# Performance work log

Hardware: AMD Instinct MI355X
Metric: run time of the kernel (lower is better)

## Reference

```python
import jax, jax.numpy as jnp
import numpy as np

B, S, D, H = 4, 2048, 1024, 16
DH = D // H


def setup_inputs() -> dict:
    key = jax.random.key(0)
    ks = jax.random.split(key, 12)
    s = 0.02
    inp = {
        "q": jax.random.normal(ks[0], (B, S, D), jnp.float32),
        "k": jax.random.normal(ks[1], (B, S, D), jnp.float32),
        "v": jax.random.normal(ks[2], (B, S, D), jnp.float32),
        # causal mask, broadcastable over batch and heads (mask==0 -> -1e9)
        "mask": jnp.tril(jnp.ones((S, S), jnp.int32))[None, None, :, :],
        "wq": jax.random.normal(ks[3], (D, D), jnp.float32) * s,
        "bq": jnp.zeros((D,), jnp.float32),
        "wk": jax.random.normal(ks[4], (D, D), jnp.float32) * s,
        "bk": jnp.zeros((D,), jnp.float32),
        "wv": jax.random.normal(ks[5], (D, D), jnp.float32) * s,
        "bv": jnp.zeros((D,), jnp.float32),
        "wo": jax.random.normal(ks[6], (D, D), jnp.float32) * s,
        "bo": jnp.zeros((D,), jnp.float32),
    }
    return inp


def reference(q, k, v, mask, wq, bq, wk, bk, wv, bv, wo, bo):
    # linear projections (torch Linear: x @ W^T + b)
    qh = (q @ wq.T + bq).reshape(B, S, H, DH).transpose(0, 2, 1, 3)  # [B,H,S,DH]
    kh = (k @ wk.T + bk).reshape(B, S, H, DH).transpose(0, 2, 1, 3)
    vh = (v @ wv.T + bv).reshape(B, S, H, DH).transpose(0, 2, 1, 3)
    scale = 1.0 / jnp.sqrt(jnp.float32(DH))
    score = jnp.einsum("bhqd,bhkd->bhqk", qh, kh) * scale  # [B,H,S,S]
    score = jnp.where(mask == 0, jnp.float32(-1e9), score)
    attn = jax.nn.softmax(score, axis=-1)
    ctx = jnp.einsum("bhqk,bhkd->bhqd", attn, vh)  # [B,H,S,DH]
    ctx = ctx.transpose(0, 2, 1, 3).reshape(B, S, D)
    return ctx @ wo.T + bo
```

## Files before the change

kernel.cpp:

```cpp
#include <hip/hip_runtime.h>
#include <hip/hip_bf16.h>

#define NB 4
#define NS 2048
#define ND 1024
#define NH 16
#define NDH 64
#define E_ 8388608
#define W_ 1048576

typedef __attribute__((ext_vector_type(8))) __bf16 bf16x8;
typedef __attribute__((ext_vector_type(4))) float f32x4;
typedef __attribute__((ext_vector_type(2))) unsigned int u32x2;
typedef unsigned short us16;
typedef unsigned int u32;

__device__ __forceinline__ unsigned short f2bf(float f) {
  union { float f; unsigned u; } v; v.f = f;
  unsigned r = v.u + 0x7FFFu + ((v.u >> 16) & 1u);
  return (unsigned short)(r >> 16);
}

typedef const __attribute__((address_space(1))) unsigned int* gas_t;
typedef __attribute__((address_space(3))) unsigned int* las_t;
__device__ __forceinline__ void gl2lds16(const void* g, void* l) {
  __builtin_amdgcn_global_load_lds((gas_t)g, (las_t)l, 16, 0, 0);
}

__global__ __launch_bounds__(256) void conv_bf16(
    const float* __restrict__ q, const float* __restrict__ k, const float* __restrict__ v,
    const float* __restrict__ wq, const float* __restrict__ wk, const float* __restrict__ wv,
    const float* __restrict__ wo,
    us16* __restrict__ qb, us16* __restrict__ kb, us16* __restrict__ vb,
    us16* __restrict__ wqb, us16* __restrict__ wkb, us16* __restrict__ wvb,
    us16* __restrict__ wob)
{
  int b = blockIdx.x;
  int seg, off;
  if (b < 24576) { seg = b >> 13; off = b & 8191; }
  else { b -= 24576; seg = 3 + (b >> 10); off = b & 1023; }
  const float* s; us16* d;
  switch (seg) {
    case 0: s = q;  d = qb;  break;
    case 1: s = k;  d = kb;  break;
    case 2: s = v;  d = vb;  break;
    case 3: s = wq; d = wqb; break;
    case 4: s = wk; d = wkb; break;
    case 5: s = wv; d = wvb; break;
    default: s = wo; d = wob; break;
  }
  size_t idx = ((size_t)off * 256 + threadIdx.x) * 4;
  float4 f = *(const float4*)(s + idx);
  ushort4 u;
  u.x = f2bf(f.x); u.y = f2bf(f.y); u.z = f2bf(f.z); u.w = f2bf(f.w);
  *(ushort4*)(d + idx) = u;
}

__global__ __launch_bounds__(256, 3) void gemm_qv(
    const us16* __restrict__ A0, const us16* __restrict__ A1,
    const us16* __restrict__ W0, const us16* __restrict__ W1,
    const float* __restrict__ bias0, const float* __restrict__ bias1,
    us16* __restrict__ out0, us16* __restrict__ out1, float scale)
{
  const int z = blockIdx.z;
  const us16* A  = z ? A1 : A0;
  const us16* Wt = z ? W1 : W0;
  const float* bias = z ? bias1 : bias0;

  __shared__ us16 As[128][64];
  __shared__ us16 Bs[128][64];
  const int tid = threadIdx.x;
  const int lane = tid & 63;
  const int w = tid >> 6;
  const int l15 = lane & 15, quad = lane >> 4;
  const int sw = l15 & 7;
  const int rowBase = blockIdx.x * 128, colBase = blockIdx.y * 128;
  const int srow = w * 32 + (lane >> 3);
  const int cu = (lane & 7) ^ ((lane >> 3) & 7);
  const us16* ga = A  + (size_t)(rowBase + srow) * ND + cu * 8;
  const us16* gb = Wt + (size_t)(colBase + srow) * ND + cu * 8;
  const int wr = (w >> 1) * 64, wc = (w & 1) * 64;

  f32x4 acc[4][4] = {};
  for (int kt = 0; kt < ND; kt += 64) {
    __syncthreads();
    #pragma unroll
    for (int c = 0; c < 4; ++c) {
      gl2lds16(ga + kt + c * 8 * ND, &As[w * 32 + c * 8][0]);
      gl2lds16(gb + kt + c * 8 * ND, &Bs[w * 32 + c * 8][0]);
    }
    __syncthreads();
    #pragma unroll
    for (int ks = 0; ks < 2; ++ks) {
      bf16x8 af[4], bfr[4];
      #pragma unroll
      for (int i = 0; i < 4; ++i)
        af[i]  = *(const bf16x8*)&As[wr + i * 16 + l15][((ks * 4 + quad) ^ sw) * 8];
      #pragma unroll
      for (int j = 0; j < 4; ++j)
        bfr[j] = *(const bf16x8*)&Bs[wc + j * 16 + l15][((ks * 4 + quad) ^ sw) * 8];
      #pragma unroll
      for (int i = 0; i < 4; ++i)
        #pragma unroll
        for (int j = 0; j < 4; ++j)
          acc[i][j] = __builtin_amdgcn_mfma_f32_16x16x32_bf16(af[i], bfr[j], acc[i][j], 0, 0, 0);
    }
  }

  if (z == 0) {
    #pragma unroll
    for (int i = 0; i < 4; ++i) {
      #pragma unroll
      for (int j = 0; j < 4; ++j) {
        int colg = colBase + wc + j * 16 + l15;
        float bval = bias[colg];
        #pragma unroll
        for (int r = 0; r < 4; ++r) {
          int rowg = rowBase + wr + i * 16 + quad * 4 + r;
          out0[(size_t)rowg * ND + colg] = f2bf((acc[i][j][r] + bval) * scale);
        }
      }
    }
  } else {
    #pragma unroll
    for (int i = 0; i < 4; ++i) {
      #pragma unroll
      for (int j = 0; j < 4; ++j) {
        int colg = colBase + wc + j * 16 + l15;
        float bval = bias[colg];
        int h_ = colg >> 6, d_ = colg & 63;
        int rowg0 = rowBase + wr + i * 16 + quad * 4;
        int b_ = rowg0 >> 11, s0 = rowg0 & (NS - 1);
        ushort4 vv;
        vv.x = f2bf(acc[i][j][0] + bval);
        vv.y = f2bf(acc[i][j][1] + bval);
        vv.z = f2bf(acc[i][j][2] + bval);
        vv.w = f2bf(acc[i][j][3] + bval);
        *(ushort4*)(out1 + ((size_t)(b_ * NH + h_) * NDH + d_) * NS + s0) = vv;
      }
    }
  }
}

__global__ __launch_bounds__(256, 4) void attn(
    const us16* __restrict__ Qh, const us16* __restrict__ Kh,
    const us16* __restrict__ Vht, us16* __restrict__ ctx)
{
  __shared__ us16 Ks[2][64][64];
  __shared__ us16 Vts[2][64][64];
  __shared__ us16 Ps[4][32][32];
  us16* Qsta = &Vts[0][0][0];

  const int bh = blockIdx.x >> 3;
  const int pr = blockIdx.x & 7;
  const int b_ = bh >> 4, h_ = bh & 15;
  const int tid = threadIdx.x, lane = tid & 63, w = tid >> 6;
  const int l15 = lane & 15, quad = lane >> 4;
  const int sw = l15 & 7;
  const int lr8 = lane >> 3;
  const int cu = (lane & 7) ^ (lr8 & 7);

  bf16x8 ones;
  #pragma unroll
  for (int i = 0; i < 8; ++i) ones[i] = (__bf16)1.0f;

  const us16* gkbase = Kh  + ((size_t)b_ * NS + w * 16 + lr8) * ND + h_ * NDH + cu * 8;
  const us16* gvbase = Vht + ((size_t)bh * NDH + w * 16 + lr8) * NS + cu * 8;

  for (int pass = 0; pass < 2; ++pass) {
    const int tq = pass ? (15 - pr) : pr;
    const int qb0 = tq * 128;
    const int nt = tq * 2 + 2;
    const int qw = qb0 + w * 32;

    __syncthreads();
    {
      const us16* gq = Qh + ((size_t)b_ * NS + qb0 + w * 32 + lr8) * ND + h_ * NDH + cu * 8;
      #pragma unroll
      for (int u = 0; u < 4; ++u)
        gl2lds16(gq + (size_t)u * 8 * ND, Qsta + (w * 32 + u * 8) * 64);
    }
    __syncthreads();
    bf16x8 bq[2][2];
    #pragma unroll
    for (int ntl = 0; ntl < 2; ++ntl)
      #pragma unroll
      for (int c = 0; c < 2; ++c)
        bq[ntl][c] = *(const bf16x8*)(Qsta + (w * 32 + ntl * 16 + l15) * 64 +
                                      (((c * 4 + quad) ^ sw) * 8));
    __syncthreads();

    gl2lds16(gkbase,            &Ks[0][w * 16][0]);
    gl2lds16(gkbase + 8 * ND,   &Ks[0][w * 16 + 8][0]);
    gl2lds16(gvbase,            &Vts[0][w * 16][0]);
    gl2lds16(gvbase + 8 * NS,   &Vts[0][w * 16 + 8][0]);

    f32x4 o[2][4] = {};
    f32x4 o_l[2] = {};

    for (int it = 0; it < nt; ++it) {
      const int kb = it * 64;
      const int cur = it & 1;
      __syncthreads();
      if (it + 1 < nt) {
        const int nxt = cur ^ 1;
        gl2lds16(gkbase + (size_t)(kb + 64) * ND,          &Ks[nxt][w * 16][0]);
        gl2lds16(gkbase + (size_t)(kb + 72) * ND,          &Ks[nxt][w * 16 + 8][0]);
        gl2lds16(gvbase + kb + 64,                         &Vts[nxt][w * 16][0]);
        gl2lds16(gvbase + kb + 64 + 8 * NS,                &Vts[nxt][w * 16 + 8][0]);
      }
      if (kb <= qw + 31) {
        const bool full = (kb + 63 <= qw);
        #pragma unroll
        for (int h2 = 0; h2 < 2; ++h2) {
          f32x4 s[2][2];
          #pragma unroll
          for (int mt = 0; mt < 2; ++mt) {
            bf16x8 ak0 = *(const bf16x8*)&Ks[cur][h2 * 32 + mt * 16 + l15][(quad ^ sw) * 8];
            bf16x8 ak1 = *(const bf16x8*)&Ks[cur][h2 * 32 + mt * 16 + l15][((4 + quad) ^ sw) * 8];
            #pragma unroll
            for (int ntl = 0; ntl < 2; ++ntl) {
              f32x4 t = {};
              t = __builtin_amdgcn_mfma_f32_16x16x32_bf16(ak0, bq[ntl][0], t, 0, 0, 0);
              t = __builtin_amdgcn_mfma_f32_16x16x32_bf16(ak1, bq[ntl][1], t, 0, 0, 0);
              s[mt][ntl] = t;
            }
          }
          #pragma unroll
          for (int mt = 0; mt < 2; ++mt)
            #pragma unroll
            for (int ntl = 0; ntl < 2; ++ntl) {
              u32 u[4];
              if (full) {
                #pragma unroll
                for (int r = 0; r < 4; ++r)
                  u[r] = __float_as_uint(__builtin_amdgcn_exp2f(s[mt][ntl][r]));
              } else {
                const int keyb = kb + h2 * 32 + mt * 16 + quad * 4;
                const int qg = qw + ntl * 16 + l15;
                #pragma unroll
                for (int r = 0; r < 4; ++r) {
                  float p = (keyb + r <= qg) ? __builtin_amdgcn_exp2f(s[mt][ntl][r]) : 0.f;
                  u[r] = __float_as_uint(p);
                }
              }
              u32 lo = (u[0] >> 16) | (u[1] & 0xffff0000u);
              u32 hi = (u[2] >> 16) | (u[3] & 0xffff0000u);
              int uswz = (mt * 2 + (quad >> 1)) ^ (l15 & 3);
              *(u32x2*)&Ps[w][ntl * 16 + l15][uswz * 8 + (quad & 1) * 4] = (u32x2){lo, hi};
            }
          #pragma unroll
          for (int ntl = 0; ntl < 2; ++ntl) {
            bf16x8 ap = *(const bf16x8*)&Ps[w][ntl * 16 + l15][(quad ^ (l15 & 3)) * 8];
            o_l[ntl] = __builtin_amdgcn_mfma_f32_16x16x32_bf16(ap, ones, o_l[ntl], 0, 0, 0);
            #pragma unroll
            for (int n = 0; n < 4; ++n) {
              bf16x8 bv = *(const bf16x8*)&Vts[cur][n * 16 + l15][((h2 * 4 + quad) ^ sw) * 8];
              o[ntl][n] = __builtin_amdgcn_mfma_f32_16x16x32_bf16(ap, bv, o[ntl][n], 0, 0, 0);
            }
          }
        }
      }
    }

    #pragma unroll
    for (int ntl = 0; ntl < 2; ++ntl) {
      #pragma unroll
      for (int r = 0; r < 4; ++r) {
        float inv = __builtin_amdgcn_rcpf(o_l[ntl][r]);
        int qg = qb0 + w * 32 + ntl * 16 + quad * 4 + r;
        us16* dst = ctx + ((size_t)b_ * NS + qg) * ND + h_ * NDH;
        #pragma unroll
        for (int n = 0; n < 4; ++n)
          dst[n * 16 + l15] = f2bf(o[ntl][n][r] * inv);
      }
    }
  }
}

__global__ __launch_bounds__(256, 3) void gemm_out(
    const us16* __restrict__ A, const us16* __restrict__ Wt,
    const float* __restrict__ bias, float* __restrict__ out)
{
  __shared__ us16 As[128][64];
  __shared__ us16 Bs[128][64];
  const int tid = threadIdx.x;
  const int lane = tid & 63;
  const int w = tid >> 6;
  const int l15 = lane & 15, quad = lane >> 4;
  const int sw = l15 & 7;
  const int rowBase = blockIdx.x * 128, colBase = blockIdx.y * 128;
  const int srow = w * 32 + (lane >> 3);
  const int cu = (lane & 7) ^ ((lane >> 3) & 7);
  const us16* ga = A  + (size_t)(rowBase + srow) * ND + cu * 8;
  const us16* gb = Wt + (size_t)(colBase + srow) * ND + cu * 8;
  const int wr = (w >> 1) * 64, wc = (w & 1) * 64;

  f32x4 acc[4][4] = {};
  for (int kt = 0; kt < ND; kt += 64) {
    __syncthreads();
    #pragma unroll
    for (int c = 0; c < 4; ++c) {
      gl2lds16(ga + kt + c * 8 * ND, &As[w * 32 + c * 8][0]);
      gl2lds16(gb + kt + c * 8 * ND, &Bs[w * 32 + c * 8][0]);
    }
    __syncthreads();
    #pragma unroll
    for (int ks = 0; ks < 2; ++ks) {
      bf16x8 af[4], bfr[4];
      #pragma unroll
      for (int i = 0; i < 4; ++i)
        af[i]  = *(const bf16x8*)&As[wr + i * 16 + l15][((ks * 4 + quad) ^ sw) * 8];
      #pragma unroll
      for (int j = 0; j < 4; ++j)
        bfr[j] = *(const bf16x8*)&Bs[wc + j * 16 + l15][((ks * 4 + quad) ^ sw) * 8];
      #pragma unroll
      for (int i = 0; i < 4; ++i)
        #pragma unroll
        for (int j = 0; j < 4; ++j)
          acc[i][j] = __builtin_amdgcn_mfma_f32_16x16x32_bf16(af[i], bfr[j], acc[i][j], 0, 0, 0);
    }
  }

  #pragma unroll
  for (int i = 0; i < 4; ++i) {
    #pragma unroll
    for (int j = 0; j < 4; ++j) {
      int colg = colBase + wc + j * 16 + l15;
      float bval = bias[colg];
      #pragma unroll
      for (int r = 0; r < 4; ++r) {
        int rowg = rowBase + wr + i * 16 + quad * 4 + r;
        out[(size_t)rowg * ND + colg] = acc[i][j][r] + bval;
      }
    }
  }
}

extern "C" void kernel_launch(void* const* d_in, const int* in_sizes, int n_in,
                              void* d_out, int out_size, void* d_ws, size_t ws_size,
                              hipStream_t stream) {
  const float* q  = (const float*)d_in[0];
  const float* k  = (const float*)d_in[1];
  const float* v  = (const float*)d_in[2];
  const float* wq = (const float*)d_in[4];
  const float* bq_ = (const float*)d_in[5];
  const float* wk = (const float*)d_in[6];
  const float* bk_ = (const float*)d_in[7];
  const float* wv = (const float*)d_in[8];
  const float* bv_ = (const float*)d_in[9];
  const float* wo = (const float*)d_in[10];
  const float* bo_ = (const float*)d_in[11];

  us16* ws = (us16*)d_ws;
  us16* qb  = ws;
  us16* kb  = ws + (size_t)E_;
  us16* vb  = ws + (size_t)2 * E_;
  us16* wqb = ws + (size_t)3 * E_;
  us16* wkb = wqb + W_;
  us16* wvb = wkb + W_;
  us16* wob = wvb + W_;
  us16* Kh  = qb;
  us16* ctx = vb;
  us16* Vht = (us16*)d_out;
  us16* Qh  = (us16*)d_out + (size_t)E_;

  const float qscale = 0.125f * 1.44269504088896340736f;

  conv_bf16<<<28672, 256, 0, stream>>>(q, k, v, wq, wk, wv, wo,
                                       qb, kb, vb, wqb, wkb, wvb, wob);
  gemm_qv<<<dim3(64, 8, 2), 256, 0, stream>>>(qb, vb, wqb, wvb, bq_, bv_,
                                              Qh, Vht, qscale);
  gemm_qv<<<dim3(64, 8, 1), 256, 0, stream>>>(kb, kb, wkb, wkb, bk_, bk_,
                                              Kh, Kh, 1.0f);
  attn<<<512, 256, 0, stream>>>(Qh, Kh, Vht, ctx);
  gemm_out<<<dim3(64, 8), 256, 0, stream>>>(ctx, wob, bo_, (float*)d_out);
}
```

Baseline: 319.9 us.

## Fuse Q/K/V projections into one launch and reorder attention block mapping

Merges the separate Q/V and K projection GEMM launches into a single three-slice grid when the workspace is large enough, writing K to a dedicated buffer instead of aliasing the Q input. This removes one kernel launch and lets all 1536 projection blocks fill the GPU together instead of running as two partly idle waves. The attention kernel also changes its block-index decode so that consecutive blocks belong to different batch-heads, spreading causal work more evenly, and it hoists the V fragment LDS reads out of the inner query-tile loop so they are reused. The fused path depends on a workspace-size check and falls back to the old two-launch sequence otherwise.

```diff
diff --git a/kernel.cpp b/kernel.cpp
--- a/kernel.cpp
+++ b/kernel.cpp
@@ -56,16 +56,19 @@
   *(ushort4*)(d + idx) = u;
 }
 
-__global__ __launch_bounds__(256, 3) void gemm_qv(
-    const us16* __restrict__ A0, const us16* __restrict__ A1,
-    const us16* __restrict__ W0, const us16* __restrict__ W1,
-    const float* __restrict__ bias0, const float* __restrict__ bias1,
-    us16* __restrict__ out0, us16* __restrict__ out1, float scale)
+__global__ __launch_bounds__(256, 3) void gemm_proj3(
+    const us16* __restrict__ A0, const us16* __restrict__ A1, const us16* __restrict__ A2,
+    const us16* __restrict__ W0, const us16* __restrict__ W1, const us16* __restrict__ W2,
+    const float* __restrict__ b0, const float* __restrict__ b1, const float* __restrict__ b2,
+    us16* __restrict__ o0, us16* __restrict__ o1, us16* __restrict__ o2,
+    float qscale, int s0, int s1, int s2)
 {
-  const int z = blockIdx.z;
-  const us16* A  = z ? A1 : A0;
-  const us16* Wt = z ? W1 : W0;
-  const float* bias = z ? bias1 : bias0;
+  const int seg = (blockIdx.z == 0) ? s0 : (blockIdx.z == 1) ? s1 : s2;
+  const us16* A  = (blockIdx.z == 0) ? A0 : (blockIdx.z == 1) ? A1 : A2;
+  const us16* Wt = (blockIdx.z == 0) ? W0 : (blockIdx.z == 1) ? W1 : W2;
+  const float* bias = (blockIdx.z == 0) ? b0 : (blockIdx.z == 1) ? b1 : b2;
+  us16* out = (blockIdx.z == 0) ? o0 : (blockIdx.z == 1) ? o1 : o2;
+  const float scale = (seg == 0) ? qscale : 1.0f;
 
   __shared__ us16 As[128][64];
   __shared__ us16 Bs[128][64];
@@ -107,7 +110,7 @@
     }
   }
 
-  if (z == 0) {
+  if (seg < 2) {
     #pragma unroll
     for (int i = 0; i < 4; ++i) {
       #pragma unroll
@@ -117,7 +120,7 @@
         #pragma unroll
         for (int r = 0; r < 4; ++r) {
           int rowg = rowBase + wr + i * 16 + quad * 4 + r;
-          out0[(size_t)rowg * ND + colg] = f2bf((acc[i][j][r] + bval) * scale);
+          out[(size_t)rowg * ND + colg] = f2bf((acc[i][j][r] + bval) * scale);
         }
       }
     }
@@ -130,13 +133,13 @@
         float bval = bias[colg];
         int h_ = colg >> 6, d_ = colg & 63;
         int rowg0 = rowBase + wr + i * 16 + quad * 4;
-        int b_ = rowg0 >> 11, s0 = rowg0 & (NS - 1);
+        int b_ = rowg0 >> 11, sr0 = rowg0 & (NS - 1);
         ushort4 vv;
         vv.x = f2bf(acc[i][j][0] + bval);
         vv.y = f2bf(acc[i][j][1] + bval);
         vv.z = f2bf(acc[i][j][2] + bval);
         vv.w = f2bf(acc[i][j][3] + bval);
-        *(ushort4*)(out1 + ((size_t)(b_ * NH + h_) * NDH + d_) * NS + s0) = vv;
+        *(ushort4*)(out + ((size_t)(b_ * NH + h_) * NDH + d_) * NS + sr0) = vv;
       }
     }
   }
@@ -151,8 +154,8 @@
   __shared__ us16 Ps[4][32][32];
   us16* Qsta = &Vts[0][0][0];
 
-  const int bh = blockIdx.x >> 3;
-  const int pr = blockIdx.x & 7;
+  const int bh = blockIdx.x & 63;
+  const int pr = blockIdx.x >> 6;
   const int b_ = bh >> 4, h_ = bh & 15;
   const int tid = threadIdx.x, lane = tid & 63, w = tid >> 6;
   const int l15 = lane & 15, quad = lane >> 4;
@@ -249,15 +252,17 @@
               int uswz = (mt * 2 + (quad >> 1)) ^ (l15 & 3);
               *(u32x2*)&Ps[w][ntl * 16 + l15][uswz * 8 + (quad & 1) * 4] = (u32x2){lo, hi};
             }
+          bf16x8 bv[4];
+          #pragma unroll
+          for (int n = 0; n < 4; ++n)
+            bv[n] = *(const bf16x8*)&Vts[cur][n * 16 + l15][((h2 * 4 + quad) ^ sw) * 8];
           #pragma unroll
           for (int ntl = 0; ntl < 2; ++ntl) {
             bf16x8 ap = *(const bf16x8*)&Ps[w][ntl * 16 + l15][(quad ^ (l15 & 3)) * 8];
             o_l[ntl] = __builtin_amdgcn_mfma_f32_16x16x32_bf16(ap, ones, o_l[ntl], 0, 0, 0);
             #pragma unroll
-            for (int n = 0; n < 4; ++n) {
-              bf16x8 bv = *(const bf16x8*)&Vts[cur][n * 16 + l15][((h2 * 4 + quad) ^ sw) * 8];
-              o[ntl][n] = __builtin_amdgcn_mfma_f32_16x16x32_bf16(ap, bv, o[ntl][n], 0, 0, 0);
-            }
+            for (int n = 0; n < 4; ++n)
+              o[ntl][n] = __builtin_amdgcn_mfma_f32_16x16x32_bf16(ap, bv[n], o[ntl][n], 0, 0, 0);
           }
         }
       }
@@ -360,19 +365,26 @@
   us16* wkb = wqb + W_;
   us16* wvb = wkb + W_;
   us16* wob = wvb + W_;
-  us16* Kh  = qb;
+  us16* KhF = wob + W_;
   us16* ctx = vb;
   us16* Vht = (us16*)d_out;
   us16* Qh  = (us16*)d_out + (size_t)E_;
 
   const float qscale = 0.125f * 1.44269504088896340736f;
+  const bool fused = ws_size >= ((size_t)4 * E_ + 4 * W_) * 2;
 
   conv_bf16<<<28672, 256, 0, stream>>>(q, k, v, wq, wk, wv, wo,
                                        qb, kb, vb, wqb, wkb, wvb, wob);
-  gemm_qv<<<dim3(64, 8, 2), 256, 0, stream>>>(qb, vb, wqb, wvb, bq_, bv_,
-                                              Qh, Vht, qscale);
-  gemm_qv<<<dim3(64, 8, 1), 256, 0, stream>>>(kb, kb, wkb, wkb, bk_, bk_,
-                                              Kh, Kh, 1.0f);
-  attn<<<512, 256, 0, stream>>>(Qh, Kh, Vht, ctx);
+  if (fused) {
+    gemm_proj3<<<dim3(64, 8, 3), 256, 0, stream>>>(
+        qb, kb, vb, wqb, wkb, wvb, bq_, bk_, bv_, Qh, KhF, Vht, qscale, 0, 1, 2);
+    attn<<<512, 256, 0, stream>>>(Qh, KhF, Vht, ctx);
+  } else {
+    gemm_proj3<<<dim3(64, 8, 2), 256, 0, stream>>>(
+        qb, vb, vb, wqb, wvb, wvb, bq_, bv_, bv_, Qh, Vht, Vht, qscale, 0, 2, 2);
+    gemm_proj3<<<dim3(64, 8, 1), 256, 0, stream>>>(
+        kb, kb, kb, wkb, wkb, wkb, bk_, bk_, bk_, qb, qb, qb, qscale, 1, 1, 1);
+    attn<<<512, 256, 0, stream>>>(Qh, qb, Vht, ctx);
+  }
   gemm_out<<<dim3(64, 8), 256, 0, stream>>>(ctx, wob, bo_, (float*)d_out);
 }
```

After: 316.7 us. Within noise of the previous version (-1.0%).
